# Kernel tuning notes

Hardware: AMD Instinct MI355X
Metric: run time of the kernel (lower is better)

Reference implementation:

```python
import jax, jax.numpy as jnp
import numpy as np

N = 100000
E = 3200000
IN_DIM = 256
HID = 128
OUT_DIM = 64


def setup_inputs() -> dict:
    key = jax.random.key(0)
    ks = jax.random.split(key, 8)
    features = jax.random.normal(ks[0], (N, IN_DIM), dtype=jnp.float32)
    edge_row = jax.random.randint(ks[1], (E,), 0, N, dtype=jnp.int32)
    edge_col = jax.random.randint(ks[2], (E,), 0, N, dtype=jnp.int32)
    edge_val = jax.random.uniform(ks[3], (E,), dtype=jnp.float32)
    W1 = jax.random.normal(ks[4], (IN_DIM, HID), dtype=jnp.float32) * (1.0 / np.sqrt(IN_DIM))
    b1 = jnp.zeros((HID,), dtype=jnp.float32)
    W2 = jax.random.normal(ks[5], (HID, OUT_DIM), dtype=jnp.float32) * (1.0 / np.sqrt(HID))
    b2 = jnp.zeros((OUT_DIM,), dtype=jnp.float32)
    return {"features": features, "edge_row": edge_row, "edge_col": edge_col,
            "edge_val": edge_val, "W1": W1, "b1": b1, "W2": W2, "b2": b2}


def reference(features, edge_row, edge_col, edge_val, W1, b1, W2, b2):
    # fc1: [N, IN_DIM] @ [IN_DIM, HID] + b1
    h = features @ W1 + b1                                   # [N, HID]
    # spmm(A, h): for each edge (r, c, v): out[r] += v * h[c]
    msgs = edge_val[:, None] * h[edge_col]                    # [E, HID] gather
    h = jax.ops.segment_sum(msgs, edge_row, num_segments=N)   # [N, HID] scatter-add
    h = jax.nn.relu(h)
    h = h @ W2 + b2                                           # [N, OUT_DIM]
    return jax.nn.log_softmax(h, axis=1)
```

## Files before the change

kernel.cpp:

```cpp
#include <hip/hip_runtime.h>
#include <math.h>

constexpr int IN_DIM  = 256;
constexpr int HID     = 128;
constexpr int OUT_DIM = 64;

constexpr int BROWS   = 128;
constexpr int NBUCK   = 782;
constexpr int CAP     = 4608;
constexpr int CHUNK   = 8192;

typedef short  bf16x8 __attribute__((ext_vector_type(8)));
typedef float  f32x4  __attribute__((ext_vector_type(4)));

__device__ __forceinline__ unsigned short f2bf(float x) {
    union { float f; unsigned u; } v; v.f = x;
    unsigned r = v.u + 0x7FFF + ((v.u >> 16) & 1);
    return (unsigned short)(r >> 16);
}

__global__ __launch_bounds__(256) void w1t_kernel(const float* __restrict__ W1,
                                                  unsigned short* __restrict__ W1T)
{
    int idx = blockIdx.x * 256 + threadIdx.x;
    int k = idx >> 7;
    int n = idx & 127;
    W1T[n * IN_DIM + k] = f2bf(W1[idx]);
}

constexpr int PADK = 264;

__global__ __launch_bounds__(256) void fc1_mfma(const float* __restrict__ feat,
                                                const unsigned short* __restrict__ W1T,
                                                const float* __restrict__ b1,
                                                unsigned short* __restrict__ h1b, int N)
{
    __shared__ unsigned short sA[64 * PADK];
    const int t    = threadIdx.x;
    const int lane = t & 63;
    const int w    = t >> 6;
    const int quad = lane >> 4;
    const int ln15 = lane & 15;
    const int row0 = blockIdx.x * 64;

#pragma unroll
    for (int i = 0; i < 16; ++i) {
        int flat = i * 256 + t;
        int r    = flat >> 6;
        int k4   = flat & 63;
        int gr   = row0 + r;
        float4 v = make_float4(0.f, 0.f, 0.f, 0.f);
        if (gr < N)
            v = *(const float4*)&feat[(size_t)gr * IN_DIM + k4 * 4];
        ushort4 o;
        o.x = f2bf(v.x); o.y = f2bf(v.y); o.z = f2bf(v.z); o.w = f2bf(v.w);
        *(ushort4*)&sA[r * PADK + k4 * 4] = o;
    }
    __syncthreads();

    f32x4 acc[8];
#pragma unroll
    for (int i = 0; i < 8; ++i) acc[i] = (f32x4){0.f, 0.f, 0.f, 0.f};

#pragma unroll
    for (int ks = 0; ks < 8; ++ks) {
        bf16x8 afrag = *(const bf16x8*)&sA[(w * 16 + ln15) * PADK + ks * 32 + quad * 8];
#pragma unroll
        for (int nt = 0; nt < 8; ++nt) {
            bf16x8 bfrag = *(const bf16x8*)&W1T[(size_t)(nt * 16 + ln15) * IN_DIM + ks * 32 + quad * 8];
            acc[nt] = __builtin_amdgcn_mfma_f32_16x16x32_bf16(afrag, bfrag, acc[nt], 0, 0, 0);
        }
    }

#pragma unroll
    for (int nt = 0; nt < 8; ++nt) {
        int col = nt * 16 + ln15;
        float bias = b1[col];
#pragma unroll
        for (int r = 0; r < 4; ++r) {
            int grow = row0 + w * 16 + quad * 4 + r;
            if (grow < N)
                h1b[(size_t)grow * HID + col] = f2bf(acc[nt][r] + bias);
        }
    }
}

__global__ __launch_bounds__(256) void bin_kernel(const int* __restrict__ erow,
                                                  const int* __restrict__ ecol,
                                                  const float* __restrict__ eval,
                                                  int* __restrict__ gCursor,
                                                  int2* __restrict__ binned, int E)
{
    __shared__ int sCnt[NBUCK];
    __shared__ int sBase[NBUCK];
    const int t = threadIdx.x;
    const int e0 = blockIdx.x * CHUNK;
    const int eEnd = min(e0 + CHUNK, E);

    for (int i = t; i < NBUCK; i += 256) sCnt[i] = 0;
    __syncthreads();

    for (int e = e0 + t; e < eEnd; e += 256)
        atomicAdd(&sCnt[erow[e] >> 7], 1);
    __syncthreads();

    for (int i = t; i < NBUCK; i += 256) {
        int c = sCnt[i];
        sBase[i] = c ? atomicAdd(&gCursor[i], c) : 0;
        sCnt[i] = 0;
    }
    __syncthreads();

    for (int e = e0 + t; e < eEnd; e += 256) {
        int   r = erow[e];
        int   c = ecol[e];
        float v = eval[e];
        int   b = r >> 7;
        int off = sBase[b] + atomicAdd(&sCnt[b], 1);
        if (off < CAP)
            binned[(size_t)b * CAP + off] = make_int2((c << 8) | ((r & 127) << 25),
                                                      __float_as_int(v));
    }
}

__global__ __launch_bounds__(256) void sort_bucket(const int* __restrict__ gCursor,
                                                   const int2* __restrict__ binned,
                                                   int2* __restrict__ edges2,
                                                   int2* __restrict__ rowIdx, int N)
{
    __shared__ int2 sEdge[CAP];
    __shared__ unsigned short sOrd[CAP];
    __shared__ int sHist[BROWS];
    __shared__ int sStart[BROWS + 1];
    __shared__ int sCur[BROWS];
    const int t  = threadIdx.x;
    const int b  = blockIdx.x;
    const int nE = min(gCursor[b], CAP);
    const size_t base = (size_t)b * CAP;

    if (t < BROWS) sHist[t] = 0;
    __syncthreads();

    for (int i = t; i < nE; i += 256) {
        int2 p = binned[base + i];
        sEdge[i] = p;
        atomicAdd(&sHist[(unsigned)p.x >> 25], 1);
    }
    __syncthreads();

    if (t < BROWS) sStart[t + 1] = sHist[t];
    if (t == 0) sStart[0] = 0;
    __syncthreads();
    for (int o = 1; o < BROWS; o <<= 1) {
        int v = 0;
        if (t < BROWS) {
            v = sStart[t + 1];
            if (t >= o) v += sStart[t + 1 - o];
        }
        __syncthreads();
        if (t < BROWS) sStart[t + 1] = v;
        __syncthreads();
    }
    if (t < BROWS) sCur[t] = sStart[t];
    __syncthreads();

    for (int i = t; i < nE; i += 256) {
        int rl = (unsigned)sEdge[i].x >> 25;
        int pos = atomicAdd(&sCur[rl], 1);
        sOrd[pos] = (unsigned short)i;
    }
    __syncthreads();

    for (int i = t; i < nE; i += 256)
        edges2[base + i] = sEdge[sOrd[i]];

    if (t < BROWS) {
        int r = b * BROWS + t;
        if (r < N)
            rowIdx[r] = make_int2((int)base + sStart[t], (int)base + sStart[t + 1]);
    }
}

__device__ __forceinline__ void accum_row(const int2* __restrict__ edges2,
                                          const char* __restrict__ h1base,
                                          int j, int jend, int lane4,
                                          float& ax, float& ay)
{
    ax = 0.f; ay = 0.f;
    for (; j + 7 < jend; j += 8) {
        int2 p[8];
#pragma unroll
        for (int u = 0; u < 8; ++u) p[u] = edges2[j + u];
        unsigned g[8];
#pragma unroll
        for (int u = 0; u < 8; ++u)
            g[u] = *(const unsigned*)(h1base + ((p[u].x & 0x01FFFFFF) + lane4));
#pragma unroll
        for (int u = 0; u < 8; ++u) {
            float v = __int_as_float(p[u].y);
            ax += v * __uint_as_float(g[u] << 16);
            ay += v * __uint_as_float(g[u] & 0xFFFF0000u);
        }
    }
    for (; j < jend; ++j) {
        int2 p = edges2[j];
        unsigned g = *(const unsigned*)(h1base + ((p.x & 0x01FFFFFF) + lane4));
        float v = __int_as_float(p.y);
        ax += v * __uint_as_float(g << 16);
        ay += v * __uint_as_float(g & 0xFFFF0000u);
    }
}

__global__ __launch_bounds__(256) void spmm_fc2_kernel(const int2* __restrict__ rowIdx,
                                                       const int2* __restrict__ edges2,
                                                       const unsigned short* __restrict__ h1b,
                                                       const float* __restrict__ W2,
                                                       const float* __restrict__ b2,
                                                       float* __restrict__ out, int N)
{
    const int lane  = threadIdx.x & 63;
    const int lane4 = lane * 4;
    const int wv    = (blockIdx.x * blockDim.x + threadIdx.x) >> 6;
    const int r0    = wv * 2;
    const int r1    = r0 + 1;
    if (r0 >= N) return;
    const char* h1base = (const char*)h1b;

    float ax0, ay0, ax1 = 0.f, ay1 = 0.f;
    int2 se0 = rowIdx[r0];
    accum_row(edges2, h1base, se0.x, se0.y, lane4, ax0, ay0);
    if (r1 < N) {
        int2 se1 = rowIdx[r1];
        accum_row(edges2, h1base, se1.x, se1.y, lane4, ax1, ay1);
    }

    ax0 = fmaxf(ax0, 0.f); ay0 = fmaxf(ay0, 0.f);
    ax1 = fmaxf(ax1, 0.f); ay1 = fmaxf(ay1, 0.f);

    float o0 = 0.f, o1 = 0.f;
#pragma unroll
    for (int j = 0; j < 64; ++j) {
        float w0 = W2[(2 * j) * OUT_DIM + lane];
        float w1 = W2[(2 * j + 1) * OUT_DIM + lane];
        o0 += __shfl(ax0, j) * w0 + __shfl(ay0, j) * w1;
        o1 += __shfl(ax1, j) * w0 + __shfl(ay1, j) * w1;
    }
    const float bias = b2[lane];
    o0 += bias; o1 += bias;

    float m0 = o0, m1 = o1;
#pragma unroll
    for (int o = 32; o > 0; o >>= 1) {
        m0 = fmaxf(m0, __shfl_xor(m0, o));
        m1 = fmaxf(m1, __shfl_xor(m1, o));
    }
    float s0 = __expf(o0 - m0), s1 = __expf(o1 - m1);
#pragma unroll
    for (int o = 32; o > 0; o >>= 1) {
        s0 += __shfl_xor(s0, o);
        s1 += __shfl_xor(s1, o);
    }
    out[(size_t)r0 * OUT_DIM + lane] = o0 - m0 - __logf(s0);
    if (r1 < N)
        out[(size_t)r1 * OUT_DIM + lane] = o1 - m1 - __logf(s1);
}

extern "C" void kernel_launch(void* const* d_in, const int* in_sizes, int n_in,
                              void* d_out, int out_size, void* d_ws, size_t ws_size,
                              hipStream_t stream) {
    const float* feat = (const float*)d_in[0];
    const int*   erow = (const int*)d_in[1];
    const int*   ecol = (const int*)d_in[2];
    const float* eval = (const float*)d_in[3];
    const float* W1   = (const float*)d_in[4];
    const float* b1   = (const float*)d_in[5];
    const float* W2   = (const float*)d_in[6];
    const float* b2   = (const float*)d_in[7];
    float*       out  = (float*)d_out;

    const int N = in_sizes[0] / IN_DIM;
    const int E = in_sizes[1];

    unsigned short* h1b    = (unsigned short*)d_ws;
    int2*           binned = (int2*)(h1b + (size_t)N * HID);
    int2*           edges2 = binned + (size_t)NBUCK * CAP;
    int2*           rowIdx = edges2 + (size_t)NBUCK * CAP;
    unsigned short* W1T    = (unsigned short*)(rowIdx + N);
    int*            gCursor= (int*)(W1T + IN_DIM * HID);

    hipMemsetAsync(gCursor, 0, NBUCK * sizeof(int), stream);

    w1t_kernel<<<(IN_DIM * HID) / 256, 256, 0, stream>>>(W1, W1T);
    fc1_mfma<<<(N + 63) / 64, 256, 0, stream>>>(feat, W1T, b1, h1b, N);
    bin_kernel<<<(E + CHUNK - 1) / CHUNK, 256, 0, stream>>>(erow, ecol, eval,
                                                            gCursor, binned, E);
    sort_bucket<<<NBUCK, 256, 0, stream>>>(gCursor, binned, edges2, rowIdx, N);

    const int nwaves = (N + 1) / 2;
    const int nblk   = (nwaves + 3) / 4;
    spmm_fc2_kernel<<<nblk, 256, 0, stream>>>(rowIdx, edges2, h1b, W2, b2, out, N);
}
```

Before: 525.0 us.

## Split fc2 into separate MFMA kernel and simplify bucket sort scatter

Result: faster. 507.1 us (-3.4%).

```diff
diff --git a/kernel.cpp b/kernel.cpp
--- a/kernel.cpp
+++ b/kernel.cpp
@@ -26,6 +26,15 @@
     int k = idx >> 7;
     int n = idx & 127;
     W1T[n * IN_DIM + k] = f2bf(W1[idx]);
+}
+
+__global__ __launch_bounds__(256) void w2t_kernel(const float* __restrict__ W2,
+                                                  unsigned short* __restrict__ W2T)
+{
+    int idx = blockIdx.x * 256 + threadIdx.x;
+    int k = idx >> 6;
+    int n = idx & 63;
+    W2T[n * HID + k] = f2bf(W2[idx]);
 }
 
 constexpr int PADK = 264;
@@ -123,13 +132,11 @@
     }
 }
 
-__global__ __launch_bounds__(256) void sort_bucket(const int* __restrict__ gCursor,
-                                                   const int2* __restrict__ binned,
-                                                   int2* __restrict__ edges2,
-                                                   int2* __restrict__ rowIdx, int N)
-{
-    __shared__ int2 sEdge[CAP];
-    __shared__ unsigned short sOrd[CAP];
+__global__ __launch_bounds__(256) void sort_bucket2(const int* __restrict__ gCursor,
+                                                    const int2* __restrict__ binned,
+                                                    int2* __restrict__ edges2,
+                                                    int2* __restrict__ rowIdx, int N)
+{
     __shared__ int sHist[BROWS];
     __shared__ int sStart[BROWS + 1];
     __shared__ int sCur[BROWS];
@@ -141,11 +148,8 @@
     if (t < BROWS) sHist[t] = 0;
     __syncthreads();
 
-    for (int i = t; i < nE; i += 256) {
-        int2 p = binned[base + i];
-        sEdge[i] = p;
-        atomicAdd(&sHist[(unsigned)p.x >> 25], 1);
-    }
+    for (int i = t; i < nE; i += 256)
+        atomicAdd(&sHist[(unsigned)binned[base + i].x >> 25], 1);
     __syncthreads();
 
     if (t < BROWS) sStart[t + 1] = sHist[t];
@@ -165,14 +169,11 @@
     __syncthreads();
 
     for (int i = t; i < nE; i += 256) {
-        int rl = (unsigned)sEdge[i].x >> 25;
+        int2 p = binned[base + i];
+        int rl = (unsigned)p.x >> 25;
         int pos = atomicAdd(&sCur[rl], 1);
-        sOrd[pos] = (unsigned short)i;
-    }
-    __syncthreads();
-
-    for (int i = t; i < nE; i += 256)
-        edges2[base + i] = sEdge[sOrd[i]];
+        edges2[base + pos] = p;
+    }
 
     if (t < BROWS) {
         int r = b * BROWS + t;
@@ -211,12 +212,10 @@
     }
 }
 
-__global__ __launch_bounds__(256) void spmm_fc2_kernel(const int2* __restrict__ rowIdx,
-                                                       const int2* __restrict__ edges2,
-                                                       const unsigned short* __restrict__ h1b,
-                                                       const float* __restrict__ W2,
-                                                       const float* __restrict__ b2,
-                                                       float* __restrict__ out, int N)
+__global__ __launch_bounds__(256) void spmm_kernel(const int2* __restrict__ rowIdx,
+                                                   const int2* __restrict__ edges2,
+                                                   const unsigned short* __restrict__ h1b,
+                                                   unsigned* __restrict__ h2b, int N)
 {
     const int lane  = threadIdx.x & 63;
     const int lane4 = lane * 4;
@@ -226,43 +225,76 @@
     if (r0 >= N) return;
     const char* h1base = (const char*)h1b;
 
-    float ax0, ay0, ax1 = 0.f, ay1 = 0.f;
+    float ax0, ay0;
     int2 se0 = rowIdx[r0];
     accum_row(edges2, h1base, se0.x, se0.y, lane4, ax0, ay0);
+    ax0 = fmaxf(ax0, 0.f); ay0 = fmaxf(ay0, 0.f);
+    h2b[(size_t)r0 * 64 + lane] = (unsigned)f2bf(ax0) | ((unsigned)f2bf(ay0) << 16);
+
     if (r1 < N) {
+        float ax1, ay1;
         int2 se1 = rowIdx[r1];
         accum_row(edges2, h1base, se1.x, se1.y, lane4, ax1, ay1);
-    }
-
-    ax0 = fmaxf(ax0, 0.f); ay0 = fmaxf(ay0, 0.f);
-    ax1 = fmaxf(ax1, 0.f); ay1 = fmaxf(ay1, 0.f);
-
-    float o0 = 0.f, o1 = 0.f;
-#pragma unroll
-    for (int j = 0; j < 64; ++j) {
-        float w0 = W2[(2 * j) * OUT_DIM + lane];
-        float w1 = W2[(2 * j + 1) * OUT_DIM + lane];
-        o0 += __shfl(ax0, j) * w0 + __shfl(ay0, j) * w1;
-        o1 += __shfl(ax1, j) * w0 + __shfl(ay1, j) * w1;
-    }
-    const float bias = b2[lane];
-    o0 += bias; o1 += bias;
-
-    float m0 = o0, m1 = o1;
-#pragma unroll
-    for (int o = 32; o > 0; o >>= 1) {
-        m0 = fmaxf(m0, __shfl_xor(m0, o));
-        m1 = fmaxf(m1, __shfl_xor(m1, o));
-    }
-    float s0 = __expf(o0 - m0), s1 = __expf(o1 - m1);
-#pragma unroll
-    for (int o = 32; o > 0; o >>= 1) {
-        s0 += __shfl_xor(s0, o);
-        s1 += __shfl_xor(s1, o);
-    }
-    out[(size_t)r0 * OUT_DIM + lane] = o0 - m0 - __logf(s0);
-    if (r1 < N)
-        out[(size_t)r1 * OUT_DIM + lane] = o1 - m1 - __logf(s1);
+        ax1 = fmaxf(ax1, 0.f); ay1 = fmaxf(ay1, 0.f);
+        h2b[(size_t)r1 * 64 + lane] = (unsigned)f2bf(ax1) | ((unsigned)f2bf(ay1) << 16);
+    }
+}
+
+__global__ __launch_bounds__(256) void fc2_mfma(const unsigned short* __restrict__ h2b,
+                                                const unsigned short* __restrict__ W2T,
+                                                const float* __restrict__ b2,
+                                                float* __restrict__ out, int N)
+{
+    const int t    = threadIdx.x;
+    const int lane = t & 63;
+    const int w    = t >> 6;
+    const int quad = lane >> 4;
+    const int ln15 = lane & 15;
+    const int row0 = blockIdx.x * 64;
+
+    int arow = row0 + w * 16 + ln15;
+    if (arow >= N) arow = N - 1;
+
+    f32x4 acc[4];
+#pragma unroll
+    for (int i = 0; i < 4; ++i) acc[i] = (f32x4){0.f, 0.f, 0.f, 0.f};
+
+#pragma unroll
+    for (int ks = 0; ks < 4; ++ks) {
+        bf16x8 afrag = *(const bf16x8*)&h2b[(size_t)arow * HID + ks * 32 + quad * 8];
+#pragma unroll
+        for (int nt = 0; nt < 4; ++nt) {
+            bf16x8 bfrag = *(const bf16x8*)&W2T[(size_t)(nt * 16 + ln15) * HID + ks * 32 + quad * 8];
+            acc[nt] = __builtin_amdgcn_mfma_f32_16x16x32_bf16(afrag, bfrag, acc[nt], 0, 0, 0);
+        }
+    }
+
+    float bias[4];
+#pragma unroll
+    for (int nt = 0; nt < 4; ++nt) bias[nt] = b2[nt * 16 + ln15];
+
+#pragma unroll
+    for (int r = 0; r < 4; ++r) {
+        float v[4];
+#pragma unroll
+        for (int nt = 0; nt < 4; ++nt) v[nt] = acc[nt][r] + bias[nt];
+
+        float m = fmaxf(fmaxf(v[0], v[1]), fmaxf(v[2], v[3]));
+#pragma unroll
+        for (int o = 1; o < 16; o <<= 1) m = fmaxf(m, __shfl_xor(m, o));
+        float s = __expf(v[0] - m) + __expf(v[1] - m) +
+                  __expf(v[2] - m) + __expf(v[3] - m);
+#pragma unroll
+        for (int o = 1; o < 16; o <<= 1) s += __shfl_xor(s, o);
+        float ls = __logf(s);
+
+        int grow = row0 + w * 16 + quad * 4 + r;
+        if (grow < N) {
+#pragma unroll
+            for (int nt = 0; nt < 4; ++nt)
+                out[(size_t)grow * OUT_DIM + nt * 16 + ln15] = v[nt] - m - ls;
+        }
+    }
 }
 
 extern "C" void kernel_launch(void* const* d_in, const int* in_sizes, int n_in,
@@ -282,21 +314,26 @@
     const int E = in_sizes[1];
 
     unsigned short* h1b    = (unsigned short*)d_ws;
-    int2*           binned = (int2*)(h1b + (size_t)N * HID);
+    unsigned short* h2b    = h1b + (size_t)N * HID;
+    int2*           binned = (int2*)(h2b + (size_t)N * HID);
     int2*           edges2 = binned + (size_t)NBUCK * CAP;
     int2*           rowIdx = edges2 + (size_t)NBUCK * CAP;
     unsigned short* W1T    = (unsigned short*)(rowIdx + N);
-    int*            gCursor= (int*)(W1T + IN_DIM * HID);
+    unsigned short* W2T    = W1T + IN_DIM * HID;
+    int*            gCursor= (int*)(W2T + HID * OUT_DIM);
 
     hipMemsetAsync(gCursor, 0, NBUCK * sizeof(int), stream);
 
     w1t_kernel<<<(IN_DIM * HID) / 256, 256, 0, stream>>>(W1, W1T);
+    w2t_kernel<<<(HID * OUT_DIM) / 256, 256, 0, stream>>>(W2, W2T);
     fc1_mfma<<<(N + 63) / 64, 256, 0, stream>>>(feat, W1T, b1, h1b, N);
     bin_kernel<<<(E + CHUNK - 1) / CHUNK, 256, 0, stream>>>(erow, ecol, eval,
                                                             gCursor, binned, E);
-    sort_bucket<<<NBUCK, 256, 0, stream>>>(gCursor, binned, edges2, rowIdx, N);
+    sort_bucket2<<<NBUCK, 256, 0, stream>>>(gCursor, binned, edges2, rowIdx, N);
 
     const int nwaves = (N + 1) / 2;
     const int nblk   = (nwaves + 3) / 4;
-    spmm_fc2_kernel<<<nblk, 256, 0, stream>>>(rowIdx, edges2, h1b, W2, b2, out, N);
-}
+    spmm_kernel<<<nblk, 256, 0, stream>>>(rowIdx, edges2, h1b,
+                                          (unsigned*)h2b, N);
+    fc2_mfma<<<(N + 63) / 64, 256, 0, stream>>>(h2b, W2T, b2, out, N);
+}
```
